# Optimization experiments

Measured on AMD Instinct MI355X. Metric: run time of the kernel, lower is better.

Reference implementation:

```python
import jax, jax.numpy as jnp
import numpy as np

N_NODES = 10000
N_EDGES = 640000
D_FEAT = 128
D_OUT = 128


def setup_inputs() -> dict:
    key = jax.random.key(0)
    k1, k2, k3, k4, k5 = jax.random.split(key, 5)
    h = jax.random.normal(k1, (N_NODES, D_FEAT), dtype=jnp.float32)
    norm = jax.random.uniform(k2, (N_NODES, 1), dtype=jnp.float32)
    # glorot-style scale for the dense weight (4*in_feats -> out_feats)
    weight = jax.random.normal(k3, (4 * D_FEAT, D_OUT), dtype=jnp.float32) * (2.0 / (4 * D_FEAT + D_OUT)) ** 0.5
    src = jax.random.randint(k4, (N_EDGES,), 0, N_NODES, dtype=jnp.int32)
    dst = jax.random.randint(k5, (N_EDGES,), 0, N_NODES, dtype=jnp.int32)
    return {"h": h, "norm": norm, "weight": weight, "src": src, "dst": dst}


def reference(h, norm, weight, src, dst):
    N = h.shape[0]
    # tf.math.l2_normalize: x * rsqrt(max(sum(x^2), 1e-12))
    h = h * jax.lax.rsqrt(jnp.maximum(jnp.sum(h * h, axis=-1, keepdims=True), 1e-12))
    h = h * norm  # [N, F]

    m = h[src]  # edge messages [E, F] (shared gather)

    # pass 1: copy_src + sum -> agg_h, then * norm
    agg_h = jax.ops.segment_sum(m, dst, num_segments=N) * norm

    # pass 2: mailbox max and mean(hard_sigmoid) over incoming messages
    deg = jax.ops.segment_sum(jnp.ones((m.shape[0],), dtype=h.dtype), dst, num_segments=N)  # [N]
    mx = jax.ops.segment_max(m, dst, num_segments=N)
    mx = jnp.where(deg[:, None] > 0, mx, 0.0)  # nodes w/o in-edges keep zeros
    # keras hard_sigmoid: clip(0.2*x + 0.5, 0, 1)
    hs_sum = jax.ops.segment_sum(jnp.clip(0.2 * m + 0.5, 0.0, 1.0), dst, num_segments=N)
    mean_hs = hs_sum / jnp.maximum(deg, 1.0)[:, None]
    accum_h = jnp.concatenate((mx, mean_hs), axis=1) * norm  # [N, 2F]

    out = jnp.concatenate((h, agg_h, accum_h), axis=1) @ weight  # [N, 4F] @ [4F, D_OUT]
    return jax.nn.relu(out)
```

## Files before the change

### kernel.cpp

```cpp
#include <hip/hip_runtime.h>
#include <math.h>

#define DF 128
#define DK 512
#define DO 128
#define CAP 128
#define CSTR 32

typedef __attribute__((ext_vector_type(8))) short bf16x8;
typedef __attribute__((ext_vector_type(8))) unsigned short u16x8;
typedef __attribute__((ext_vector_type(4))) float f32x4;

__device__ inline unsigned short f2bf(float x) {
    unsigned int u = __builtin_bit_cast(unsigned int, x);
    unsigned int r = (u + 0x7FFFu + ((u >> 16) & 1u)) >> 16;
    return (unsigned short)r;
}
__device__ inline float bf2f(unsigned short b) {
    unsigned int u = ((unsigned int)b) << 16;
    return __builtin_bit_cast(float, u);
}
__device__ inline float hsig(float v) {
    return fminf(fmaxf(0.2f * v + 0.5f, 0.0f), 1.0f);
}

__global__ void wt_k(const float* __restrict__ W, unsigned short* __restrict__ Wt) {
    int t = blockIdx.x * blockDim.x + threadIdx.x;
    int c  = t >> 6;
    int k0 = (t & 63) * 8;
    u16x8 v;
    #pragma unroll
    for (int j = 0; j < 8; ++j) v[j] = f2bf(W[(size_t)(k0 + j) * DO + c]);
    *reinterpret_cast<u16x8*>(Wt + (size_t)c * DK + k0) = v;
}

__global__ void normalize_k(const float* __restrict__ h,
                            const float* __restrict__ norm,
                            unsigned short* __restrict__ Xb,
                            int* __restrict__ cur, int N) {
    int wid = threadIdx.x >> 6;
    int t   = threadIdx.x & 63;
    int n   = blockIdx.x * 4 + wid;
    if (n >= N) return;
    if (t == 0) cur[(size_t)n * CSTR] = 0;
    const float2 hv = reinterpret_cast<const float2*>(h + (size_t)n * DF)[t];
    float ss = hv.x * hv.x + hv.y * hv.y;
    #pragma unroll
    for (int o = 32; o > 0; o >>= 1) ss += __shfl_xor(ss, o);
    float scale = rsqrtf(fmaxf(ss, 1e-12f)) * norm[n];
    ushort2 o2;
    o2.x = f2bf(hv.x * scale);
    o2.y = f2bf(hv.y * scale);
    reinterpret_cast<ushort2*>(Xb + (size_t)n * DK)[t] = o2;
}

__global__ void bucket_k(const int* __restrict__ src, const int* __restrict__ dst,
                         int* __restrict__ cur, unsigned short* __restrict__ bsrc, int E) {
    int t  = blockIdx.x * blockDim.x + threadIdx.x;
    int e0 = t * 4;
    if (e0 + 3 < E) {
        const int4 d4 = *reinterpret_cast<const int4*>(dst + e0);
        const int4 s4 = *reinterpret_cast<const int4*>(src + e0);
        int p0 = atomicAdd(&cur[(size_t)d4.x * CSTR], 1);
        int p1 = atomicAdd(&cur[(size_t)d4.y * CSTR], 1);
        int p2 = atomicAdd(&cur[(size_t)d4.z * CSTR], 1);
        int p3 = atomicAdd(&cur[(size_t)d4.w * CSTR], 1);
        if (p0 < CAP) bsrc[((size_t)d4.x << 7) + p0] = (unsigned short)s4.x;
        if (p1 < CAP) bsrc[((size_t)d4.y << 7) + p1] = (unsigned short)s4.y;
        if (p2 < CAP) bsrc[((size_t)d4.z << 7) + p2] = (unsigned short)s4.z;
        if (p3 < CAP) bsrc[((size_t)d4.w << 7) + p3] = (unsigned short)s4.w;
    } else {
        for (int e = e0; e < E; ++e) {
            int d = dst[e];
            int p = atomicAdd(&cur[(size_t)d * CSTR], 1);
            if (p < CAP) bsrc[((size_t)d << 7) + p] = (unsigned short)src[e];
        }
    }
}

__global__ void gather_k(unsigned short* __restrict__ Xb,
                         const int* __restrict__ cur,
                         const float* __restrict__ norm,
                         const unsigned short* __restrict__ bsrc, int N) {
    int n = blockIdx.x;
    int t = threadIdx.x;
    int cnt = min(cur[(size_t)n * CSTR], CAP);
    __shared__ int sid[CAP];
    unsigned int pr = reinterpret_cast<const unsigned int*>(bsrc + ((size_t)n << 7))[t];
    sid[2 * t]     = (int)(pr & 0xFFFFu);
    sid[2 * t + 1] = (int)(pr >> 16);
    __syncthreads();
    int f0 = t * 2;
    float s0 = 0.f, s1 = 0.f, hs0 = 0.f, hs1 = 0.f;
    float mx0 = -INFINITY, mx1 = -INFINITY;
    int j = 0;
    for (; j + 2 <= cnt; j += 2) {
        unsigned int va = *reinterpret_cast<const unsigned int*>(Xb + (size_t)sid[j]     * DK + f0);
        unsigned int vb = *reinterpret_cast<const unsigned int*>(Xb + (size_t)sid[j + 1] * DK + f0);
        float a0 = bf2f((unsigned short)(va & 0xFFFFu)), a1 = bf2f((unsigned short)(va >> 16));
        float b0 = bf2f((unsigned short)(vb & 0xFFFFu)), b1 = bf2f((unsigned short)(vb >> 16));
        s0 += a0 + b0;  s1 += a1 + b1;
        mx0 = fmaxf(mx0, fmaxf(a0, b0));  mx1 = fmaxf(mx1, fmaxf(a1, b1));
        hs0 += hsig(a0) + hsig(b0);  hs1 += hsig(a1) + hsig(b1);
    }
    for (; j < cnt; ++j) {
        unsigned int va = *reinterpret_cast<const unsigned int*>(Xb + (size_t)sid[j] * DK + f0);
        float a0 = bf2f((unsigned short)(va & 0xFFFFu)), a1 = bf2f((unsigned short)(va >> 16));
        s0 += a0;  s1 += a1;
        mx0 = fmaxf(mx0, a0);  mx1 = fmaxf(mx1, a1);
        hs0 += hsig(a0);  hs1 += hsig(a1);
    }
    if (cnt == 0) { mx0 = 0.f; mx1 = 0.f; }
    float nm  = norm[n];
    float inv = 1.0f / fmaxf((float)cnt, 1.0f);
    size_t row = (size_t)n * DK;
    unsigned int o;
    o = (unsigned int)f2bf(s0 * nm)        | ((unsigned int)f2bf(s1 * nm) << 16);
    *reinterpret_cast<unsigned int*>(Xb + row + 128 + f0) = o;
    o = (unsigned int)f2bf(mx0 * nm)       | ((unsigned int)f2bf(mx1 * nm) << 16);
    *reinterpret_cast<unsigned int*>(Xb + row + 256 + f0) = o;
    o = (unsigned int)f2bf(hs0 * inv * nm) | ((unsigned int)f2bf(hs1 * inv * nm) << 16);
    *reinterpret_cast<unsigned int*>(Xb + row + 384 + f0) = o;
}

__global__ void gemm_k(const unsigned short* __restrict__ Xb,
                       const unsigned short* __restrict__ Wt,
                       float* __restrict__ out, int N) {
    int row0 = blockIdx.x * 16;
    int l = threadIdx.x;
    int r  = l & 15;
    int kg = l >> 4;
    f32x4 acc[8] = {};
    const bf16x8* Arow = reinterpret_cast<const bf16x8*>(Xb + (size_t)(row0 + r) * DK);
    #pragma unroll 4
    for (int ks = 0; ks < 16; ++ks) {
        bf16x8 a = Arow[ks * 4 + kg];
        #pragma unroll
        for (int nb = 0; nb < 8; ++nb) {
            const bf16x8* Bp = reinterpret_cast<const bf16x8*>(Wt + (size_t)(nb * 16 + r) * DK);
            bf16x8 b = Bp[ks * 4 + kg];
            acc[nb] = __builtin_amdgcn_mfma_f32_16x16x32_bf16(a, b, acc[nb], 0, 0, 0);
        }
    }
    #pragma unroll
    for (int nb = 0; nb < 8; ++nb) {
        #pragma unroll
        for (int q = 0; q < 4; ++q) {
            int rr = row0 + kg * 4 + q;
            if (rr < N) out[(size_t)rr * DO + nb * 16 + r] = fmaxf(acc[nb][q], 0.0f);
        }
    }
}

extern "C" void kernel_launch(void* const* d_in, const int* in_sizes, int n_in,
                              void* d_out, int out_size, void* d_ws, size_t ws_size,
                              hipStream_t stream) {
    const float* h    = (const float*)d_in[0];
    const float* norm = (const float*)d_in[1];
    const float* W    = (const float*)d_in[2];
    const int*   src  = (const int*)d_in[3];
    const int*   dst  = (const int*)d_in[4];
    float* out = (float*)d_out;

    int N = in_sizes[0] / DF;
    int E = in_sizes[3];

    unsigned short* Xb = (unsigned short*)d_ws;
    unsigned short* Wt = Xb + (size_t)N * DK;
    int* cur = (int*)(Wt + (size_t)DO * DK);
    unsigned short* bsrc = (unsigned short*)(cur + (size_t)N * CSTR);

    wt_k       <<<dim3(32),                dim3(256), 0, stream>>>(W, Wt);
    normalize_k<<<dim3((N + 3) / 4),       dim3(256), 0, stream>>>(h, norm, Xb, cur, N);
    bucket_k   <<<dim3((E / 4 + 255)/256), dim3(256), 0, stream>>>(src, dst, cur, bsrc, E);
    gather_k   <<<dim3(N),                 dim3(64),  0, stream>>>(Xb, cur, norm, bsrc, N);
    gemm_k     <<<dim3((N + 15) / 16),     dim3(64),  0, stream>>>(Xb, Wt, out, N);
}
```

Baseline: 84.22 us.

## Fuse neighbor aggregation with GEMM via LDS staging and merge prep kernels

Merges the weight-transpose and normalize kernels into one launch. Replaces the separate gather and GEMM kernels with one 256-thread kernel per 16 nodes: each wave aggregates 4 nodes into shared memory, and the block then runs the bf16 MFMA GEMM straight from LDS. This avoids writing the aggregated features to global memory and reading them back, and cuts two kernel launches. The cost is fewer in-flight waves during the latency-bound gather, since each wave now processes four nodes one after another. The mean divisor now uses the uncapped degree.

Result: faster. 81.43 us (-3.3%).

```diff
diff --git a/kernel.cpp b/kernel.cpp
--- a/kernel.cpp
+++ b/kernel.cpp
@@ -24,34 +24,34 @@
     return fminf(fmaxf(0.2f * v + 0.5f, 0.0f), 1.0f);
 }
 
-__global__ void wt_k(const float* __restrict__ W, unsigned short* __restrict__ Wt) {
-    int t = blockIdx.x * blockDim.x + threadIdx.x;
-    int c  = t >> 6;
-    int k0 = (t & 63) * 8;
-    u16x8 v;
-    #pragma unroll
-    for (int j = 0; j < 8; ++j) v[j] = f2bf(W[(size_t)(k0 + j) * DO + c]);
-    *reinterpret_cast<u16x8*>(Wt + (size_t)c * DK + k0) = v;
-}
-
-__global__ void normalize_k(const float* __restrict__ h,
-                            const float* __restrict__ norm,
-                            unsigned short* __restrict__ Xb,
-                            int* __restrict__ cur, int N) {
-    int wid = threadIdx.x >> 6;
-    int t   = threadIdx.x & 63;
-    int n   = blockIdx.x * 4 + wid;
-    if (n >= N) return;
-    if (t == 0) cur[(size_t)n * CSTR] = 0;
-    const float2 hv = reinterpret_cast<const float2*>(h + (size_t)n * DF)[t];
-    float ss = hv.x * hv.x + hv.y * hv.y;
-    #pragma unroll
-    for (int o = 32; o > 0; o >>= 1) ss += __shfl_xor(ss, o);
-    float scale = rsqrtf(fmaxf(ss, 1e-12f)) * norm[n];
-    ushort2 o2;
-    o2.x = f2bf(hv.x * scale);
-    o2.y = f2bf(hv.y * scale);
-    reinterpret_cast<ushort2*>(Xb + (size_t)n * DK)[t] = o2;
+__global__ void prep_k(const float* __restrict__ W, unsigned short* __restrict__ Wt,
+                       const float* __restrict__ h, const float* __restrict__ norm,
+                       unsigned short* __restrict__ Xb, int* __restrict__ cur, int N) {
+    int b = blockIdx.x;
+    if (b < 32) {
+        int t = b * 256 + threadIdx.x;
+        int c  = t >> 6;
+        int k0 = (t & 63) * 8;
+        u16x8 v;
+        #pragma unroll
+        for (int j = 0; j < 8; ++j) v[j] = f2bf(W[(size_t)(k0 + j) * DO + c]);
+        *reinterpret_cast<u16x8*>(Wt + (size_t)c * DK + k0) = v;
+    } else {
+        int wid = threadIdx.x >> 6;
+        int t   = threadIdx.x & 63;
+        int n   = (b - 32) * 4 + wid;
+        if (n >= N) return;
+        if (t == 0) cur[(size_t)n * CSTR] = 0;
+        const float2 hv = reinterpret_cast<const float2*>(h + (size_t)n * DF)[t];
+        float ss = hv.x * hv.x + hv.y * hv.y;
+        #pragma unroll
+        for (int o = 32; o > 0; o >>= 1) ss += __shfl_xor(ss, o);
+        float scale = rsqrtf(fmaxf(ss, 1e-12f)) * norm[n];
+        ushort2 o2;
+        o2.x = f2bf(hv.x * scale);
+        o2.y = f2bf(hv.y * scale);
+        reinterpret_cast<ushort2*>(Xb + (size_t)n * DK)[t] = o2;
+    }
 }
 
 __global__ void bucket_k(const int* __restrict__ src, const int* __restrict__ dst,
@@ -78,76 +78,90 @@
     }
 }
 
-__global__ void gather_k(unsigned short* __restrict__ Xb,
-                         const int* __restrict__ cur,
-                         const float* __restrict__ norm,
-                         const unsigned short* __restrict__ bsrc, int N) {
-    int n = blockIdx.x;
-    int t = threadIdx.x;
-    int cnt = min(cur[(size_t)n * CSTR], CAP);
-    __shared__ int sid[CAP];
-    unsigned int pr = reinterpret_cast<const unsigned int*>(bsrc + ((size_t)n << 7))[t];
-    sid[2 * t]     = (int)(pr & 0xFFFFu);
-    sid[2 * t + 1] = (int)(pr >> 16);
+__global__ void __launch_bounds__(256) fused_k(const unsigned short* __restrict__ Xb,
+                                               const unsigned short* __restrict__ Wt,
+                                               const int* __restrict__ cur,
+                                               const float* __restrict__ norm,
+                                               const unsigned short* __restrict__ bsrc,
+                                               float* __restrict__ out, int N) {
+    __shared__ unsigned short Xs[16][520];
+    __shared__ unsigned short sid[16][128];
+    int tid = threadIdx.x;
+    int w = tid >> 6;
+    int l = tid & 63;
+    int nb0 = blockIdx.x * 16;
+    int rg = l >> 5;
+    int lc = l & 31;
+
+    for (int i = 0; i < 4; ++i) {
+        int ni = w * 4 + i;
+        int n  = nb0 + ni;
+        if (n >= N) continue;
+        int cntt = cur[(size_t)n * CSTR];
+        int cnt  = min(cntt, CAP);
+        reinterpret_cast<unsigned int*>(&sid[ni][0])[l] =
+            reinterpret_cast<const unsigned int*>(bsrc + ((size_t)n << 7))[l];
+        if (l < 32)
+            reinterpret_cast<ushort4*>(&Xs[ni][0])[lc] =
+                reinterpret_cast<const ushort4*>(Xb + (size_t)n * DK)[lc];
+
+        float s0 = 0.f, s1 = 0.f, s2 = 0.f, s3 = 0.f;
+        float h0 = 0.f, h1 = 0.f, h2 = 0.f, h3 = 0.f;
+        float m0 = -INFINITY, m1 = -INFINITY, m2 = -INFINITY, m3 = -INFINITY;
+        #pragma unroll 2
+        for (int j = rg; j < cnt; j += 2) {
+            int sj = (int)sid[ni][j];
+            ushort4 v = *reinterpret_cast<const ushort4*>(Xb + (size_t)sj * DK + lc * 4);
+            float a0 = bf2f(v.x), a1 = bf2f(v.y), a2 = bf2f(v.z), a3 = bf2f(v.w);
+            s0 += a0; s1 += a1; s2 += a2; s3 += a3;
+            m0 = fmaxf(m0, a0); m1 = fmaxf(m1, a1); m2 = fmaxf(m2, a2); m3 = fmaxf(m3, a3);
+            h0 += hsig(a0); h1 += hsig(a1); h2 += hsig(a2); h3 += hsig(a3);
+        }
+        s0 += __shfl_xor(s0, 32); s1 += __shfl_xor(s1, 32);
+        s2 += __shfl_xor(s2, 32); s3 += __shfl_xor(s3, 32);
+        h0 += __shfl_xor(h0, 32); h1 += __shfl_xor(h1, 32);
+        h2 += __shfl_xor(h2, 32); h3 += __shfl_xor(h3, 32);
+        m0 = fmaxf(m0, __shfl_xor(m0, 32)); m1 = fmaxf(m1, __shfl_xor(m1, 32));
+        m2 = fmaxf(m2, __shfl_xor(m2, 32)); m3 = fmaxf(m3, __shfl_xor(m3, 32));
+
+        if (l < 32) {
+            float nm  = norm[n];
+            float inv = 1.0f / fmaxf((float)cntt, 1.0f);
+            ushort4 o;
+            o.x = f2bf(s0 * nm); o.y = f2bf(s1 * nm);
+            o.z = f2bf(s2 * nm); o.w = f2bf(s3 * nm);
+            *reinterpret_cast<ushort4*>(&Xs[ni][128 + lc * 4]) = o;
+            float q0 = (cnt > 0) ? m0 : 0.f, q1 = (cnt > 0) ? m1 : 0.f;
+            float q2 = (cnt > 0) ? m2 : 0.f, q3 = (cnt > 0) ? m3 : 0.f;
+            o.x = f2bf(q0 * nm); o.y = f2bf(q1 * nm);
+            o.z = f2bf(q2 * nm); o.w = f2bf(q3 * nm);
+            *reinterpret_cast<ushort4*>(&Xs[ni][256 + lc * 4]) = o;
+            o.x = f2bf(h0 * inv * nm); o.y = f2bf(h1 * inv * nm);
+            o.z = f2bf(h2 * inv * nm); o.w = f2bf(h3 * inv * nm);
+            *reinterpret_cast<ushort4*>(&Xs[ni][384 + lc * 4]) = o;
+        }
+    }
     __syncthreads();
-    int f0 = t * 2;
-    float s0 = 0.f, s1 = 0.f, hs0 = 0.f, hs1 = 0.f;
-    float mx0 = -INFINITY, mx1 = -INFINITY;
-    int j = 0;
-    for (; j + 2 <= cnt; j += 2) {
-        unsigned int va = *reinterpret_cast<const unsigned int*>(Xb + (size_t)sid[j]     * DK + f0);
-        unsigned int vb = *reinterpret_cast<const unsigned int*>(Xb + (size_t)sid[j + 1] * DK + f0);
-        float a0 = bf2f((unsigned short)(va & 0xFFFFu)), a1 = bf2f((unsigned short)(va >> 16));
-        float b0 = bf2f((unsigned short)(vb & 0xFFFFu)), b1 = bf2f((unsigned short)(vb >> 16));
-        s0 += a0 + b0;  s1 += a1 + b1;
-        mx0 = fmaxf(mx0, fmaxf(a0, b0));  mx1 = fmaxf(mx1, fmaxf(a1, b1));
-        hs0 += hsig(a0) + hsig(b0);  hs1 += hsig(a1) + hsig(b1);
-    }
-    for (; j < cnt; ++j) {
-        unsigned int va = *reinterpret_cast<const unsigned int*>(Xb + (size_t)sid[j] * DK + f0);
-        float a0 = bf2f((unsigned short)(va & 0xFFFFu)), a1 = bf2f((unsigned short)(va >> 16));
-        s0 += a0;  s1 += a1;
-        mx0 = fmaxf(mx0, a0);  mx1 = fmaxf(mx1, a1);
-        hs0 += hsig(a0);  hs1 += hsig(a1);
-    }
-    if (cnt == 0) { mx0 = 0.f; mx1 = 0.f; }
-    float nm  = norm[n];
-    float inv = 1.0f / fmaxf((float)cnt, 1.0f);
-    size_t row = (size_t)n * DK;
-    unsigned int o;
-    o = (unsigned int)f2bf(s0 * nm)        | ((unsigned int)f2bf(s1 * nm) << 16);
-    *reinterpret_cast<unsigned int*>(Xb + row + 128 + f0) = o;
-    o = (unsigned int)f2bf(mx0 * nm)       | ((unsigned int)f2bf(mx1 * nm) << 16);
-    *reinterpret_cast<unsigned int*>(Xb + row + 256 + f0) = o;
-    o = (unsigned int)f2bf(hs0 * inv * nm) | ((unsigned int)f2bf(hs1 * inv * nm) << 16);
-    *reinterpret_cast<unsigned int*>(Xb + row + 384 + f0) = o;
-}
 
-__global__ void gemm_k(const unsigned short* __restrict__ Xb,
-                       const unsigned short* __restrict__ Wt,
-                       float* __restrict__ out, int N) {
-    int row0 = blockIdx.x * 16;
-    int l = threadIdx.x;
     int r  = l & 15;
     int kg = l >> 4;
-    f32x4 acc[8] = {};
-    const bf16x8* Arow = reinterpret_cast<const bf16x8*>(Xb + (size_t)(row0 + r) * DK);
-    #pragma unroll 4
+    f32x4 acc0 = {}, acc1 = {};
+    const unsigned short* B0 = Wt + (size_t)(w * 32 + r) * DK;
+    const unsigned short* B1 = Wt + (size_t)(w * 32 + 16 + r) * DK;
+    #pragma unroll
     for (int ks = 0; ks < 16; ++ks) {
-        bf16x8 a = Arow[ks * 4 + kg];
-        #pragma unroll
-        for (int nb = 0; nb < 8; ++nb) {
-            const bf16x8* Bp = reinterpret_cast<const bf16x8*>(Wt + (size_t)(nb * 16 + r) * DK);
-            bf16x8 b = Bp[ks * 4 + kg];
-            acc[nb] = __builtin_amdgcn_mfma_f32_16x16x32_bf16(a, b, acc[nb], 0, 0, 0);
-        }
+        bf16x8 a  = *reinterpret_cast<const bf16x8*>(&Xs[r][ks * 32 + kg * 8]);
+        bf16x8 b0 = *reinterpret_cast<const bf16x8*>(B0 + ks * 32 + kg * 8);
+        bf16x8 b1 = *reinterpret_cast<const bf16x8*>(B1 + ks * 32 + kg * 8);
+        acc0 = __builtin_amdgcn_mfma_f32_16x16x32_bf16(a, b0, acc0, 0, 0, 0);
+        acc1 = __builtin_amdgcn_mfma_f32_16x16x32_bf16(a, b1, acc1, 0, 0, 0);
     }
     #pragma unroll
-    for (int nb = 0; nb < 8; ++nb) {
-        #pragma unroll
-        for (int q = 0; q < 4; ++q) {
-            int rr = row0 + kg * 4 + q;
-            if (rr < N) out[(size_t)rr * DO + nb * 16 + r] = fmaxf(acc[nb][q], 0.0f);
+    for (int q = 0; q < 4; ++q) {
+        int rr = nb0 + kg * 4 + q;
+        if (rr < N) {
+            out[(size_t)rr * DO + w * 32 + r]      = fmaxf(acc0[q], 0.0f);
+            out[(size_t)rr * DO + w * 32 + 16 + r] = fmaxf(acc1[q], 0.0f);
         }
     }
 }
@@ -170,9 +184,8 @@
     int* cur = (int*)(Wt + (size_t)DO * DK);
     unsigned short* bsrc = (unsigned short*)(cur + (size_t)N * CSTR);
 
-    wt_k       <<<dim3(32),                dim3(256), 0, stream>>>(W, Wt);
-    normalize_k<<<dim3((N + 3) / 4),       dim3(256), 0, stream>>>(h, norm, Xb, cur, N);
-    bucket_k   <<<dim3((E / 4 + 255)/256), dim3(256), 0, stream>>>(src, dst, cur, bsrc, E);
-    gather_k   <<<dim3(N),                 dim3(64),  0, stream>>>(Xb, cur, norm, bsrc, N);
-    gemm_k     <<<dim3((N + 15) / 16),     dim3(64),  0, stream>>>(Xb, Wt, out, N);
+    int nblk = (N + 3) / 4 + 32;
+    prep_k  <<<dim3(nblk),              dim3(256), 0, stream>>>(W, Wt, h, norm, Xb, cur, N);
+    bucket_k<<<dim3((E / 4 + 255)/256), dim3(256), 0, stream>>>(src, dst, cur, bsrc, E);
+    fused_k <<<dim3((N + 15) / 16),     dim3(256), 0, stream>>>(Xb, Wt, cur, norm, bsrc, out, N);
 }
```
